# Performance work log

Measured on AMD Instinct MI355X. Metric: run time of the kernel, lower is better.

The kernel has to match this reference:

```python
import jax, jax.numpy as jnp
import numpy as np

N = 100000      # nodes
E = 1600000     # edges (before self-loops)
F_IN = 16       # num_node_features
HID = 16        # hid
HEADS = 4       # in_head == out_head
B = 64          # num graphs
G = 16          # num_global_features
NEG_SLOPE = 0.2


def gat_conv(x, src, dst, W, a_src, a_dst, b, concat):
    """PyG-style GATConv. x:[N,F], W:[F,H*C], a_src/a_dst:[H,C], b:[H*C] or [C]."""
    n = x.shape[0]
    H, C = a_src.shape
    h = (x @ W).reshape(n, H, C)                       # [N,H,C]
    alpha_s = (h * a_src).sum(-1)                      # [N,H]
    alpha_d = (h * a_dst).sum(-1)                      # [N,H]
    e = jax.nn.leaky_relu(alpha_s[src] + alpha_d[dst], NEG_SLOPE)  # [E',H]
    # segment softmax over destination nodes (stable; max is grad-free)
    m = jax.lax.stop_gradient(jax.ops.segment_max(e, dst, num_segments=n))
    ex = jnp.exp(e - m[dst])
    denom = jax.ops.segment_sum(ex, dst, num_segments=n)
    alpha = ex / (denom[dst] + 1e-16)                  # [E',H]
    out = jax.ops.segment_sum(h[src] * alpha[:, :, None], dst, num_segments=n)  # [N,H,C]
    out = out.reshape(n, H * C) if concat else out.mean(axis=1)
    return out + b


def setup_inputs() -> dict:
    key = jax.random.key(0)
    ks = jax.random.split(key, 24)
    s = 0.1
    inp = {
        "x": jax.random.normal(ks[0], (N, F_IN), jnp.float32),
        "stats": jax.random.normal(ks[1], (B, G), jnp.float32),
        # conv1: F_IN -> HID, heads=HEADS, concat=True
        "W1": jax.random.normal(ks[2], (F_IN, HEADS * HID), jnp.float32) * s,
        "a1s": jax.random.normal(ks[3], (HEADS, HID), jnp.float32) * s,
        "a1d": jax.random.normal(ks[4], (HEADS, HID), jnp.float32) * s,
        "b1": jnp.zeros((HEADS * HID,), jnp.float32),
        # conv2: HID*HEADS -> HID, heads=HEADS, concat=False
        "W2": jax.random.normal(ks[5], (HEADS * HID, HEADS * HID), jnp.float32) * s,
        "a2s": jax.random.normal(ks[6], (HEADS, HID), jnp.float32) * s,
        "a2d": jax.random.normal(ks[7], (HEADS, HID), jnp.float32) * s,
        "b2": jnp.zeros((HID,), jnp.float32),
        # conv3: HID -> HID, heads=HEADS, concat=False
        "W3": jax.random.normal(ks[8], (HID, HEADS * HID), jnp.float32) * s,
        "a3s": jax.random.normal(ks[9], (HEADS, HID), jnp.float32) * s,
        "a3d": jax.random.normal(ks[10], (HEADS, HID), jnp.float32) * s,
        "b3": jnp.zeros((HID,), jnp.float32),
        # MLP head
        "fw1": jax.random.normal(ks[11], (HID + G, 32), jnp.float32) * s,
        "fb1": jnp.zeros((32,), jnp.float32),
        "fw2": jax.random.normal(ks[12], (32, 16), jnp.float32) * s,
        "fb2": jnp.zeros((16,), jnp.float32),
        "fw3": jax.random.normal(ks[13], (16, 1), jnp.float32) * s,
        "fb3": jnp.zeros((1,), jnp.float32),
        "edge_index": jax.random.randint(ks[14], (2, E), 0, N, jnp.int64),
        "batch": jnp.sort(jax.random.randint(ks[15], (N,), 0, B, jnp.int64)),
    }
    return inp


def reference(x, stats, W1, a1s, a1d, b1, W2, a2s, a2d, b2, W3, a3s, a3d, b3,
              fw1, fb1, fw2, fb2, fw3, fb3, edge_index, batch):
    n = x.shape[0]
    loops = jnp.arange(n, dtype=edge_index.dtype)
    src = jnp.concatenate([edge_index[0], loops])  # add_self_loops=True (PyG default)
    dst = jnp.concatenate([edge_index[1], loops])
    h = jax.nn.elu(gat_conv(x, src, dst, W1, a1s, a1d, b1, True))
    h = jax.nn.elu(gat_conv(h, src, dst, W2, a2s, a2d, b2, False))
    h = gat_conv(h, src, dst, W3, a3s, a3d, b3, False)
    nb = stats.shape[0]
    pooled = jax.ops.segment_sum(h, batch, num_segments=nb)
    counts = jax.ops.segment_sum(jnp.ones((n,), h.dtype), batch, num_segments=nb)
    pooled = pooled / jnp.maximum(counts, 1.0)[:, None]   # global_mean_pool
    z = jnp.concatenate([pooled, stats], axis=1)
    z = jax.nn.relu(z @ fw1 + fb1)
    z = jax.nn.relu(z @ fw2 + fb2)
    return z @ fw3 + fb3
```

## Files before the change

### kernel.cpp

```cpp
#include <hip/hip_runtime.h>
#include <hip/hip_bf16.h>
#include <hip/hip_fp16.h>

#define NNODES 100000
#define NEDGES 1600000
#define NHEADS 4
#define NHID   16
#define NB     64
#define NG     16
#define POOL_BLOCKS 128
#define POOL_SLOTS (NB * NG + NB)

#define BKT_SHIFT 7
#define NPB 128
#define NBKT ((NNODES + NPB - 1) / NPB)
#define BCAP 4096

__device__ __forceinline__ float leaky02(float v) {
    return v > 0.0f ? v : 0.2f * v;
}

__device__ __forceinline__ float4 loadH4(const __half* p) {
    uint2 raw = *(const uint2*)p;
    __half2 a = *reinterpret_cast<const __half2*>(&raw.x);
    __half2 b = *reinterpret_cast<const __half2*>(&raw.y);
    float2 fa = __half22float2(a), fb = __half22float2(b);
    return make_float4(fa.x, fa.y, fb.x, fb.y);
}

template <int FIN>
__global__ void node_linear3(const float* __restrict__ X,
                             const float* __restrict__ W,
                             const float* __restrict__ a_s,
                             const float* __restrict__ a_d,
                             __half* __restrict__ H,
                             float* __restrict__ AS,
                             float* __restrict__ AD, int n) {
    int lane = threadIdx.x & 63;
    int head = lane >> 4;
    int wave = __builtin_amdgcn_readfirstlane(
        (int)((blockIdx.x * blockDim.x + threadIdx.x) >> 6));
    int nwaves = (gridDim.x * blockDim.x) >> 6;

    float w[FIN];
#pragma unroll
    for (int k = 0; k < FIN; ++k) w[k] = W[k * 64 + lane];
    float asl = a_s[lane], adl = a_d[lane];

    for (int i = wave; i < n; i += nwaves) {
        const float* __restrict__ xr = X + (size_t)i * FIN;
        float acc = 0.0f;
#pragma unroll
        for (int k = 0; k < FIN; ++k) acc += xr[k] * w[k];
        H[(size_t)i * 64 + lane] = __float2half_rn(acc);
        float s1 = acc * asl, s2 = acc * adl;
#pragma unroll
        for (int off = 1; off < 16; off <<= 1) {
            s1 += __shfl_xor(s1, off);
            s2 += __shfl_xor(s2, off);
        }
        if ((lane & 15) == 0) {
            AS[(size_t)i * 4 + head] = s1;
            AD[(size_t)i * 4 + head] = s2;
        }
    }
}

__global__ void bucket_scatter(const int* __restrict__ src,
                               const int* __restrict__ dst,
                               int* __restrict__ bucketCnt,
                               unsigned int* __restrict__ pairs, int ne) {
    __shared__ int hist[NBKT];
    __shared__ int base[NBKT];
    int tid = threadIdx.x;
    for (int i = tid; i < NBKT; i += 256) hist[i] = 0;
    __syncthreads();

    int chunk = (ne + gridDim.x - 1) / gridDim.x;
    int beg = blockIdx.x * chunk;
    int end = min(beg + chunk, ne);

    for (int e = beg + tid; e < end; e += 256)
        atomicAdd(&hist[dst[e] >> BKT_SHIFT], 1);
    __syncthreads();

    for (int i = tid; i < NBKT; i += 256) {
        int h = hist[i];
        base[i] = h ? atomicAdd(&bucketCnt[i], h) : 0;
        hist[i] = 0;
    }
    __syncthreads();

    for (int e = beg + tid; e < end; e += 256) {
        int d = dst[e];
        int bkt = d >> BKT_SHIFT;
        int r = base[bkt] + atomicAdd(&hist[bkt], 1);
        if (r < BCAP)
            pairs[(size_t)bkt * BCAP + r] =
                (unsigned)src[e] | ((unsigned)(d & (NPB - 1)) << 20);
    }
}

__global__ void bucket_scan(const int* __restrict__ bucketCnt,
                            int* __restrict__ bucketOff,
                            int* __restrict__ indptr, int n) {
    __shared__ int sd[1024];
    int t = threadIdx.x;
    int v = (t < NBKT) ? min(bucketCnt[t], BCAP) : 0;
    sd[t] = v;
    __syncthreads();
    for (int off = 1; off < 1024; off <<= 1) {
        int x = (t >= off) ? sd[t - off] : 0;
        __syncthreads();
        if (t >= off) sd[t] += x;
        __syncthreads();
    }
    if (t < NBKT) bucketOff[t] = sd[t] - v;
    if (t == NBKT - 1) {
        bucketOff[NBKT] = sd[t];
        indptr[n] = sd[t];
    }
}

__global__ void bucket_sort(const unsigned int* __restrict__ pairs,
                            const int* __restrict__ bucketCnt,
                            const int* __restrict__ bucketOff,
                            int* __restrict__ srcs,
                            int* __restrict__ indptr, int n) {
    __shared__ int hist[NPB];
    __shared__ int offl[NPB];
    __shared__ int cur[NPB];
    __shared__ int lsrc[BCAP];
    int bkt = blockIdx.x;
    int t = threadIdx.x;
    int cnt = min(bucketCnt[bkt], BCAP);
    int boff = bucketOff[bkt];
    if (t < NPB) hist[t] = 0;
    __syncthreads();

    const unsigned int* __restrict__ p = pairs + (size_t)bkt * BCAP;
    unsigned int v[BCAP / 256];
#pragma unroll
    for (int i = 0; i < BCAP / 256; ++i) {
        int e = i * 256 + t;
        v[i] = 0u;
        if (e < cnt) {
            v[i] = p[e];
            atomicAdd(&hist[v[i] >> 20], 1);
        }
    }
    __syncthreads();
    if (t < NPB) offl[t] = hist[t];
    __syncthreads();
    for (int off = 1; off < NPB; off <<= 1) {
        int x = 0;
        if (t < NPB && t >= off) x = offl[t - off];
        __syncthreads();
        if (t < NPB && t >= off) offl[t] += x;
        __syncthreads();
    }
    if (t < NPB) {
        int ex = offl[t] - hist[t];
        cur[t] = ex;
        int node = bkt * NPB + t;
        if (node < n) indptr[node] = boff + ex;
    }
    __syncthreads();
#pragma unroll
    for (int i = 0; i < BCAP / 256; ++i) {
        int e = i * 256 + t;
        if (e < cnt) {
            int r = atomicAdd(&cur[v[i] >> 20], 1);
            lsrc[r] = (int)(v[i] & 0xFFFFFu);
        }
    }
    __syncthreads();
    for (int e = t; e < cnt; e += 256) srcs[boff + e] = lsrc[e];
}

template <int MODE>
__global__ void gat_pull2(const __half* __restrict__ H,
                          const float* __restrict__ AS,
                          const float* __restrict__ AD,
                          const int* __restrict__ indptr,
                          const int* __restrict__ srcs,
                          const float* __restrict__ bias,
                          float* __restrict__ out, int n) {
    int lane = threadIdx.x & 63;
    int grp  = lane >> 4;
    int sl   = lane & 15;
    int head = sl >> 2;
    int wave = (blockIdx.x * blockDim.x + threadIdx.x) >> 6;
    int nwaves = (gridDim.x * blockDim.x) >> 6;

    for (int d = wave; d < n; d += nwaves) {
        float ad = AD[(size_t)d * 4 + head];
        float4 acc = {0.f, 0.f, 0.f, 0.f};
        float den = 0.0f;
        if (grp == 0) {
            float t = AS[(size_t)d * 4 + head] + ad;
            float w = __expf(t > 0.f ? t : 0.2f * t);
            den = w;
            float4 h4 = loadH4(H + (size_t)d * 64 + sl * 4);
            acc.x = w * h4.x; acc.y = w * h4.y;
            acc.z = w * h4.z; acc.w = w * h4.w;
        }
        int beg = indptr[d], end = indptr[d + 1];
        for (int e0 = beg; e0 < end; e0 += 64) {
            int cnt = min(64, end - e0);
            int myS = (lane < cnt) ? srcs[e0 + lane] : 0;
            int j = 0;
            for (; j + 16 <= cnt; j += 16) {
                int s[4]; float a[4]; float4 h4[4];
#pragma unroll
                for (int q = 0; q < 4; ++q)
                    s[q] = __shfl(myS, j + q * 4 + grp);
#pragma unroll
                for (int q = 0; q < 4; ++q)
                    a[q] = AS[(size_t)s[q] * 4 + head];
#pragma unroll
                for (int q = 0; q < 4; ++q)
                    h4[q] = loadH4(H + (size_t)s[q] * 64 + sl * 4);
#pragma unroll
                for (int q = 0; q < 4; ++q) {
                    float t = a[q] + ad;
                    float w = __expf(t > 0.f ? t : 0.2f * t);
                    den += w;
                    acc.x += w * h4[q].x; acc.y += w * h4[q].y;
                    acc.z += w * h4[q].z; acc.w += w * h4[q].w;
                }
            }
            for (; j < cnt; j += 4) {
                int idx = j + grp;
                int s = __shfl(myS, idx & 63);
                if (idx < cnt) {
                    float t = AS[(size_t)s * 4 + head] + ad;
                    float w = __expf(t > 0.f ? t : 0.2f * t);
                    den += w;
                    float4 h4 = loadH4(H + (size_t)s * 64 + sl * 4);
                    acc.x += w * h4.x; acc.y += w * h4.y;
                    acc.z += w * h4.z; acc.w += w * h4.w;
                }
            }
        }
#pragma unroll
        for (int off = 16; off < 64; off <<= 1) {
            acc.x += __shfl_xor(acc.x, off);
            acc.y += __shfl_xor(acc.y, off);
            acc.z += __shfl_xor(acc.z, off);
            acc.w += __shfl_xor(acc.w, off);
            den   += __shfl_xor(den, off);
        }
        float inv = 1.0f / (den + 1e-16f);
        float4 v = {acc.x * inv, acc.y * inv, acc.z * inv, acc.w * inv};
        if (MODE == 0) {
            if (grp == 0) {
                float4 b4 = *(const float4*)(bias + sl * 4);
                v.x += b4.x; v.y += b4.y; v.z += b4.z; v.w += b4.w;
                v.x = v.x > 0.f ? v.x : __expf(v.x) - 1.f;
                v.y = v.y > 0.f ? v.y : __expf(v.y) - 1.f;
                v.z = v.z > 0.f ? v.z : __expf(v.z) - 1.f;
                v.w = v.w > 0.f ? v.w : __expf(v.w) - 1.f;
                *(float4*)(out + (size_t)d * 64 + sl * 4) = v;
            }
        } else {
#pragma unroll
            for (int off = 4; off <= 8; off <<= 1) {
                v.x += __shfl_xor(v.x, off);
                v.y += __shfl_xor(v.y, off);
                v.z += __shfl_xor(v.z, off);
                v.w += __shfl_xor(v.w, off);
            }
            float4 b4 = *(const float4*)(bias + (sl & 3) * 4);
            v.x = 0.25f * v.x + b4.x; v.y = 0.25f * v.y + b4.y;
            v.z = 0.25f * v.z + b4.z; v.w = 0.25f * v.w + b4.w;
            if (MODE == 1) {
                v.x = v.x > 0.f ? v.x : __expf(v.x) - 1.f;
                v.y = v.y > 0.f ? v.y : __expf(v.y) - 1.f;
                v.z = v.z > 0.f ? v.z : __expf(v.z) - 1.f;
                v.w = v.w > 0.f ? v.w : __expf(v.w) - 1.f;
            }
            if (grp == 0 && sl < 4)
                *(float4*)(out + (size_t)d * 16 + sl * 4) = v;
        }
    }
}

__global__ void pool_stage1(const float* __restrict__ Hf,
                            const int* __restrict__ batch,
                            float* __restrict__ partials, int n) {
    __shared__ float lp[POOL_SLOTS];
    int tid = threadIdx.x;
    for (int i = tid; i < POOL_SLOTS; i += 256) lp[i] = 0.0f;
    __syncthreads();

    int chunk = (n + POOL_BLOCKS - 1) / POOL_BLOCKS;
    int start = blockIdx.x * chunk;
    int end = min(start + chunk, n);
    int c = tid & 15;
    for (int node = start + (tid >> 4); node < end; node += 16) {
        int b = batch[node];
        atomicAdd(&lp[b * 16 + c], Hf[(size_t)node * 16 + c]);
        if (c == 0) atomicAdd(&lp[NB * NG + b], 1.0f);
    }
    __syncthreads();
    float* outp = partials + (size_t)blockIdx.x * POOL_SLOTS;
    for (int i = tid; i < POOL_SLOTS; i += 256) outp[i] = lp[i];
}

__global__ void pool_stage2(const float* __restrict__ partials,
                            float* __restrict__ pooled_counts) {
    int idx = blockIdx.x * blockDim.x + threadIdx.x;
    if (idx >= POOL_SLOTS) return;
    float s = 0.0f;
    for (int j = 0; j < POOL_BLOCKS; ++j)
        s += partials[(size_t)j * POOL_SLOTS + idx];
    pooled_counts[idx] = s;
}

__global__ void mlp_head(const float* __restrict__ pooled_counts,
                         const float* __restrict__ stats,
                         const float* __restrict__ fw1, const float* __restrict__ fb1,
                         const float* __restrict__ fw2, const float* __restrict__ fb2,
                         const float* __restrict__ fw3, const float* __restrict__ fb3,
                         float* __restrict__ out) {
    int g = threadIdx.x;
    if (g >= NB) return;
    const float* pooled = pooled_counts;
    const float* counts = pooled_counts + NB * NG;
    float z[32];
    float inv = 1.0f / fmaxf(counts[g], 1.0f);
#pragma unroll
    for (int c = 0; c < 16; ++c) z[c] = pooled[g * 16 + c] * inv;
#pragma unroll
    for (int c = 0; c < 16; ++c) z[16 + c] = stats[g * 16 + c];

    float z1[32];
#pragma unroll
    for (int j = 0; j < 32; ++j) {
        float acc = fb1[j];
        for (int k = 0; k < 32; ++k) acc += z[k] * fw1[k * 32 + j];
        z1[j] = fmaxf(acc, 0.0f);
    }
    float z2[16];
#pragma unroll
    for (int j = 0; j < 16; ++j) {
        float acc = fb2[j];
        for (int k = 0; k < 32; ++k) acc += z1[k] * fw2[k * 16 + j];
        z2[j] = fmaxf(acc, 0.0f);
    }
    float acc = fb3[0];
#pragma unroll
    for (int k = 0; k < 16; ++k) acc += z2[k] * fw3[k];
    out[g] = acc;
}

extern "C" void kernel_launch(void* const* d_in, const int* in_sizes, int n_in,
                              void* d_out, int out_size, void* d_ws, size_t ws_size,
                              hipStream_t stream) {
    const float* x    = (const float*)d_in[0];
    const float* stats= (const float*)d_in[1];
    const float* W1   = (const float*)d_in[2];
    const float* a1s  = (const float*)d_in[3];
    const float* a1d  = (const float*)d_in[4];
    const float* b1   = (const float*)d_in[5];
    const float* W2   = (const float*)d_in[6];
    const float* a2s  = (const float*)d_in[7];
    const float* a2d  = (const float*)d_in[8];
    const float* b2   = (const float*)d_in[9];
    const float* W3   = (const float*)d_in[10];
    const float* a3s  = (const float*)d_in[11];
    const float* a3d  = (const float*)d_in[12];
    const float* b3   = (const float*)d_in[13];
    const float* fw1  = (const float*)d_in[14];
    const float* fb1  = (const float*)d_in[15];
    const float* fw2  = (const float*)d_in[16];
    const float* fb2  = (const float*)d_in[17];
    const float* fw3  = (const float*)d_in[18];
    const float* fb3  = (const float*)d_in[19];
    const int* ei     = (const int*)d_in[20];
    const int* batch  = (const int*)d_in[21];

    const int n = NNODES, ne = NEDGES;
    const int* srcI = ei;
    const int* dstI = ei + ne;

    float* ws = (float*)d_ws;
    __half* Hh  = (__half*)ws;
    float* B    = (float*)(Hh + (size_t)n * 64);
    float* C2   = B + (size_t)n * 64;
    float* AS   = C2 + (size_t)n * 16;
    float* AD   = AS + (size_t)n * 4;
    float* PC   = AD + (size_t)n * 4;
    float* PART = PC + POOL_SLOTS;
    int* bucketCnt = (int*)(PART + (size_t)POOL_BLOCKS * POOL_SLOTS);
    int* bucketOff = bucketCnt + NBKT;
    int* indptr    = bucketOff + NBKT + 1;
    int* srcs      = indptr + n + 1;
    unsigned int* pairs = (unsigned int*)B;

    const int TB = 256;
    const int nlBlocks   = 2048;
    const int pullBlocks = 2048;

    hipMemsetAsync(bucketCnt, 0, NBKT * sizeof(int), stream);
    bucket_scatter<<<512, TB, 0, stream>>>(srcI, dstI, bucketCnt, pairs, ne);
    bucket_scan<<<1, 1024, 0, stream>>>(bucketCnt, bucketOff, indptr, n);
    bucket_sort<<<NBKT, TB, 0, stream>>>(pairs, bucketCnt, bucketOff, srcs,
                                         indptr, n);

    node_linear3<16><<<nlBlocks, TB, 0, stream>>>(x, W1, a1s, a1d, Hh, AS, AD, n);
    gat_pull2<0><<<pullBlocks, TB, 0, stream>>>(Hh, AS, AD, indptr, srcs, b1, B, n);

    node_linear3<64><<<nlBlocks, TB, 0, stream>>>(B, W2, a2s, a2d, Hh, AS, AD, n);
    gat_pull2<1><<<pullBlocks, TB, 0, stream>>>(Hh, AS, AD, indptr, srcs, b2, C2, n);

    node_linear3<16><<<nlBlocks, TB, 0, stream>>>(C2, W3, a3s, a3d, Hh, AS, AD, n);
    gat_pull2<2><<<pullBlocks, TB, 0, stream>>>(Hh, AS, AD, indptr, srcs, b3, B, n);

    pool_stage1<<<POOL_BLOCKS, TB, 0, stream>>>(B, batch, PART, n);
    pool_stage2<<<(POOL_SLOTS + TB - 1) / TB, TB, 0, stream>>>(PART, PC);
    mlp_head<<<1, 64, 0, stream>>>(PC, stats, fw1, fb1, fw2, fb2, fw3, fb3,
                                   (float*)d_out);
}
```

Before: 396.5 us.

## Process four destination nodes per wave in GAT pull kernel

Reworks the GAT aggregation so each 16-lane group of a wave owns its own destination node, instead of the whole wave splitting one node's edges four ways. This removes the cross-group shuffle reduction and idle lanes on low-degree nodes, and the grid is resized to cover every node once. In exchange, groups within a wave diverge when neighboring nodes have unequal degrees, and each group handles 4 edges per unrolled step instead of 16.

```diff
diff --git a/kernel.cpp b/kernel.cpp
--- a/kernel.cpp
+++ b/kernel.cpp
@@ -179,7 +179,7 @@
 }
 
 template <int MODE>
-__global__ void gat_pull2(const __half* __restrict__ H,
+__global__ void gat_pull3(const __half* __restrict__ H,
                           const float* __restrict__ AS,
                           const float* __restrict__ AD,
                           const int* __restrict__ indptr,
@@ -193,47 +193,45 @@
     int wave = (blockIdx.x * blockDim.x + threadIdx.x) >> 6;
     int nwaves = (gridDim.x * blockDim.x) >> 6;
 
-    for (int d = wave; d < n; d += nwaves) {
-        float ad = AD[(size_t)d * 4 + head];
-        float4 acc = {0.f, 0.f, 0.f, 0.f};
-        float den = 0.0f;
-        if (grp == 0) {
-            float t = AS[(size_t)d * 4 + head] + ad;
-            float w = __expf(t > 0.f ? t : 0.2f * t);
-            den = w;
-            float4 h4 = loadH4(H + (size_t)d * 64 + sl * 4);
-            acc.x = w * h4.x; acc.y = w * h4.y;
-            acc.z = w * h4.z; acc.w = w * h4.w;
-        }
-        int beg = indptr[d], end = indptr[d + 1];
-        for (int e0 = beg; e0 < end; e0 += 64) {
-            int cnt = min(64, end - e0);
-            int myS = (lane < cnt) ? srcs[e0 + lane] : 0;
-            int j = 0;
-            for (; j + 16 <= cnt; j += 16) {
-                int s[4]; float a[4]; float4 h4[4];
-#pragma unroll
-                for (int q = 0; q < 4; ++q)
-                    s[q] = __shfl(myS, j + q * 4 + grp);
-#pragma unroll
-                for (int q = 0; q < 4; ++q)
-                    a[q] = AS[(size_t)s[q] * 4 + head];
-#pragma unroll
-                for (int q = 0; q < 4; ++q)
-                    h4[q] = loadH4(H + (size_t)s[q] * 64 + sl * 4);
-#pragma unroll
-                for (int q = 0; q < 4; ++q) {
-                    float t = a[q] + ad;
-                    float w = __expf(t > 0.f ? t : 0.2f * t);
-                    den += w;
-                    acc.x += w * h4[q].x; acc.y += w * h4[q].y;
-                    acc.z += w * h4[q].z; acc.w += w * h4[q].w;
+    for (int d0 = wave * 4; d0 < n; d0 += nwaves * 4) {
+        int d = d0 + grp;
+        if (d < n) {
+            float ad  = AD[(size_t)d * 4 + head];
+            float asd = AS[(size_t)d * 4 + head];
+            float t0 = asd + ad;
+            float wself = __expf(t0 > 0.f ? t0 : 0.2f * t0);
+            float den = wself;
+            float4 h4s = loadH4(H + (size_t)d * 64 + sl * 4);
+            float4 acc = {wself * h4s.x, wself * h4s.y,
+                          wself * h4s.z, wself * h4s.w};
+
+            int beg = indptr[d], end = indptr[d + 1];
+            for (int e0 = beg; e0 < end; e0 += 16) {
+                int cnt = min(16, end - e0);
+                int myS = (sl < cnt) ? srcs[e0 + sl] : 0;
+                int j = 0;
+                for (; j + 4 <= cnt; j += 4) {
+                    int s[4]; float a[4]; float4 h4[4];
+#pragma unroll
+                    for (int q = 0; q < 4; ++q)
+                        s[q] = __shfl(myS, (grp << 4) + j + q);
+#pragma unroll
+                    for (int q = 0; q < 4; ++q)
+                        a[q] = AS[(size_t)s[q] * 4 + head];
+#pragma unroll
+                    for (int q = 0; q < 4; ++q)
+                        h4[q] = loadH4(H + (size_t)s[q] * 64 + sl * 4);
+#pragma unroll
+                    for (int q = 0; q < 4; ++q) {
+                        float t = a[q] + ad;
+                        float w = __expf(t > 0.f ? t : 0.2f * t);
+                        den += w;
+                        acc.x += w * h4[q].x; acc.y += w * h4[q].y;
+                        acc.z += w * h4[q].z; acc.w += w * h4[q].w;
+                    }
                 }
-            }
-            for (; j < cnt; j += 4) {
-                int idx = j + grp;
-                int s = __shfl(myS, idx & 63);
-                if (idx < cnt) {
+                for (; j < cnt; ++j) {
+                    int s = __shfl(myS, (grp << 4) + j);
                     float t = AS[(size_t)s * 4 + head] + ad;
                     float w = __expf(t > 0.f ? t : 0.2f * t);
                     den += w;
@@ -242,19 +240,9 @@
                     acc.z += w * h4.z; acc.w += w * h4.w;
                 }
             }
-        }
-#pragma unroll
-        for (int off = 16; off < 64; off <<= 1) {
-            acc.x += __shfl_xor(acc.x, off);
-            acc.y += __shfl_xor(acc.y, off);
-            acc.z += __shfl_xor(acc.z, off);
-            acc.w += __shfl_xor(acc.w, off);
-            den   += __shfl_xor(den, off);
-        }
-        float inv = 1.0f / (den + 1e-16f);
-        float4 v = {acc.x * inv, acc.y * inv, acc.z * inv, acc.w * inv};
-        if (MODE == 0) {
-            if (grp == 0) {
+            float inv = 1.0f / (den + 1e-16f);
+            float4 v = {acc.x * inv, acc.y * inv, acc.z * inv, acc.w * inv};
+            if (MODE == 0) {
                 float4 b4 = *(const float4*)(bias + sl * 4);
                 v.x += b4.x; v.y += b4.y; v.z += b4.z; v.w += b4.w;
                 v.x = v.x > 0.f ? v.x : __expf(v.x) - 1.f;
@@ -262,26 +250,26 @@
                 v.z = v.z > 0.f ? v.z : __expf(v.z) - 1.f;
                 v.w = v.w > 0.f ? v.w : __expf(v.w) - 1.f;
                 *(float4*)(out + (size_t)d * 64 + sl * 4) = v;
+            } else {
+#pragma unroll
+                for (int off = 4; off <= 8; off <<= 1) {
+                    v.x += __shfl_xor(v.x, off);
+                    v.y += __shfl_xor(v.y, off);
+                    v.z += __shfl_xor(v.z, off);
+                    v.w += __shfl_xor(v.w, off);
+                }
+                float4 b4 = *(const float4*)(bias + (sl & 3) * 4);
+                v.x = 0.25f * v.x + b4.x; v.y = 0.25f * v.y + b4.y;
+                v.z = 0.25f * v.z + b4.z; v.w = 0.25f * v.w + b4.w;
+                if (MODE == 1) {
+                    v.x = v.x > 0.f ? v.x : __expf(v.x) - 1.f;
+                    v.y = v.y > 0.f ? v.y : __expf(v.y) - 1.f;
+                    v.z = v.z > 0.f ? v.z : __expf(v.z) - 1.f;
+                    v.w = v.w > 0.f ? v.w : __expf(v.w) - 1.f;
+                }
+                if (sl < 4)
+                    *(float4*)(out + (size_t)d * 16 + sl * 4) = v;
             }
-        } else {
-#pragma unroll
-            for (int off = 4; off <= 8; off <<= 1) {
-                v.x += __shfl_xor(v.x, off);
-                v.y += __shfl_xor(v.y, off);
-                v.z += __shfl_xor(v.z, off);
-                v.w += __shfl_xor(v.w, off);
-            }
-            float4 b4 = *(const float4*)(bias + (sl & 3) * 4);
-            v.x = 0.25f * v.x + b4.x; v.y = 0.25f * v.y + b4.y;
-            v.z = 0.25f * v.z + b4.z; v.w = 0.25f * v.w + b4.w;
-            if (MODE == 1) {
-                v.x = v.x > 0.f ? v.x : __expf(v.x) - 1.f;
-                v.y = v.y > 0.f ? v.y : __expf(v.y) - 1.f;
-                v.z = v.z > 0.f ? v.z : __expf(v.z) - 1.f;
-                v.w = v.w > 0.f ? v.w : __expf(v.w) - 1.f;
-            }
-            if (grp == 0 && sl < 4)
-                *(float4*)(out + (size_t)d * 16 + sl * 4) = v;
         }
     }
 }
@@ -401,7 +389,7 @@
 
     const int TB = 256;
     const int nlBlocks   = 2048;
-    const int pullBlocks = 2048;
+    const int pullBlocks = (n + 15) / 16;
 
     hipMemsetAsync(bucketCnt, 0, NBKT * sizeof(int), stream);
     bucket_scatter<<<512, TB, 0, stream>>>(srcI, dstI, bucketCnt, pairs, ne);
@@ -410,13 +398,13 @@
                                          indptr, n);
 
     node_linear3<16><<<nlBlocks, TB, 0, stream>>>(x, W1, a1s, a1d, Hh, AS, AD, n);
-    gat_pull2<0><<<pullBlocks, TB, 0, stream>>>(Hh, AS, AD, indptr, srcs, b1, B, n);
+    gat_pull3<0><<<pullBlocks, TB, 0, stream>>>(Hh, AS, AD, indptr, srcs, b1, B, n);
 
     node_linear3<64><<<nlBlocks, TB, 0, stream>>>(B, W2, a2s, a2d, Hh, AS, AD, n);
-    gat_pull2<1><<<pullBlocks, TB, 0, stream>>>(Hh, AS, AD, indptr, srcs, b2, C2, n);
+    gat_pull3<1><<<pullBlocks, TB, 0, stream>>>(Hh, AS, AD, indptr, srcs, b2, C2, n);
 
     node_linear3<16><<<nlBlocks, TB, 0, stream>>>(C2, W3, a3s, a3d, Hh, AS, AD, n);
-    gat_pull2<2><<<pullBlocks, TB, 0, stream>>>(Hh, AS, AD, indptr, srcs, b3, B, n);
+    gat_pull3<2><<<pullBlocks, TB, 0, stream>>>(Hh, AS, AD, indptr, srcs, b3, B, n);
 
     pool_stage1<<<POOL_BLOCKS, TB, 0, stream>>>(B, batch, PART, n);
     pool_stage2<<<(POOL_SLOTS + TB - 1) / TB, TB, 0, stream>>>(PART, PC);
```

After: 373.2 us. 1.06x faster.
